# Kernel tuning notes

Hardware: AMD Instinct MI355X
Metric: run time of the kernel (lower is better)

Reference implementation:

```python
import jax, jax.numpy as jnp
import numpy as np

B, S, D, H, MLP, RH, RANK, BS, E, RES = 64, 197, 768, 12, 3072, 512, 256, 2, 3, 1
EPS = 1e-5


def _ln(x, g, b):
    m = jnp.mean(x, -1, keepdims=True)
    v = jnp.mean((x - m) ** 2, -1, keepdims=True)
    return (x - m) / jnp.sqrt(v + EPS) * g + b


def setup_inputs() -> dict:
    key = jax.random.key(0)
    ks = jax.random.split(key, 16)
    n = lambda k, shp, s: (jax.random.normal(k, shp) * s).astype(jnp.float32)
    inp = {
        'x': n(ks[0], (B, S, D), 1.0),
        'LRA_mask': jnp.arange(2 ** BS, dtype=jnp.int32),
        'wq_w': n(ks[1], (D, D), 0.02), 'wq_b': jnp.zeros((D,), jnp.float32),
        'wk_w': n(ks[2], (D, D), 0.02), 'wk_b': jnp.zeros((D,), jnp.float32),
        'wv_w': n(ks[3], (D, D), 0.02), 'wv_b': jnp.zeros((D,), jnp.float32),
        'wo_w': n(ks[4], (D, D), 0.02), 'wo_b': jnp.zeros((D,), jnp.float32),
        'an_g': jnp.ones((D,), jnp.float32), 'an_b': jnp.zeros((D,), jnp.float32),
        'fc1_w': n(ks[5], (MLP, D), 0.02), 'fc1_b': jnp.zeros((MLP,), jnp.float32),
        'fc2_w': n(ks[6], (D, MLP), 0.02), 'fc2_b': jnp.zeros((D,), jnp.float32),
        'fn_g': jnp.ones((D,), jnp.float32), 'fn_b': jnp.zeros((D,), jnp.float32),
        'r1_w': n(ks[7], (RH, D), 0.01), 'r1_b': jnp.zeros((RH,), jnp.float32),
        'rn_g': jnp.ones((RH,), jnp.float32), 'rn_b': jnp.zeros((RH,), jnp.float32),
        'r2_w': n(ks[8], (BS * 2, RH), 0.01),
        'r2_b': jnp.array([0.1, 5.0] * BS, jnp.float32),
        'eA': n(ks[9], (E, RANK, D), 0.01),  # down_proj weights [out=rank, in=dim]
        'eB': n(ks[10], (E, D, RANK), 0.01),  # up_proj weights [out=dim, in=rank]
    }
    return inp


def reference(x, LRA_mask, wq_w, wq_b, wk_w, wk_b, wv_w, wv_b, wo_w, wo_b,
              an_g, an_b, fc1_w, fc1_b, fc2_w, fc2_b, fn_g, fn_b,
              r1_w, r1_b, rn_g, rn_b, r2_w, r2_b, eA, eB):
    hd = D // H
    # ---- RouterModule (eval mode: argmax hard routing) on block input ----
    rlog = jax.nn.silu(_ln(x @ r1_w.T + r1_b, rn_g, rn_b)) @ r2_w.T + r2_b
    rlog = rlog.reshape(B, S, BS, 2)
    bits = jnp.argmax(rlog, -1)               # [B,S,BS], value of channel-1 one-hot
    bits = bits.at[:, :RES, :].set(1)          # reserved tokens -> full-one key (identity)
    pw = 2 ** jnp.arange(BS - 1, -1, -1)
    idx = jnp.sum(bits * pw, -1)               # [B,S] routing key per token
    # ---- Attention (pre-norm) ----
    h = _ln(x, an_g, an_b)
    q = (h @ wq_w.T + wq_b).reshape(B, S, H, hd).transpose(0, 2, 1, 3)
    k = (h @ wk_w.T + wk_b).reshape(B, S, H, hd).transpose(0, 2, 1, 3)
    v = (h @ wv_w.T + wv_b).reshape(B, S, H, hd).transpose(0, 2, 1, 3)
    att = jax.nn.softmax(jnp.einsum('bhqd,bhkd->bhqk', q, k) / np.float32(np.sqrt(hd)), -1)
    o = jnp.einsum('bhqk,bhkd->bhqd', att, v).transpose(0, 2, 1, 3).reshape(B, S, D)
    x1 = x + (o @ wo_w.T + wo_b)
    # ---- FeedForward (pre-norm, exact GELU like torch nn.GELU) ----
    x2 = x1 + (jax.nn.gelu(_ln(x1, fn_g, fn_b) @ fc1_w.T + fc1_b, approximate=False) @ fc2_w.T + fc2_b)
    # ---- BlockPathApproximators: disjoint per-key residual LoRA experts ----
    # keys 0..E-1 have experts; key 2^BS-1 (full-one) is identity. LRA_mask covers all keys.
    down = jnp.einsum('bsd,erd->bser', x2, eA)            # [B,S,E,RANK]
    up = jnp.einsum('bser,edr->bsed', down, eB)           # [B,S,E,D]
    sel = (idx[..., None] == jnp.arange(E)).astype(x2.dtype)  # one-hot over experts [B,S,E]
    out = x2 + jnp.einsum('bsed,bse->bsd', up, sel)
    return out
```

## Files before the change

### kernel.cpp

```cpp
#include <hip/hip_runtime.h>
#include <cstdint>

#define B_SZ   64
#define SEQ    197
#define DIM    768
#define NHEAD  12
#define HDK    64
#define MLP_D  3072
#define RH_D   512
#define RANK_D 256
#define NEXP   3
#define TOK    (B_SZ*SEQ)

typedef unsigned short u16;
typedef __attribute__((ext_vector_type(8))) short s16x8;
typedef __attribute__((ext_vector_type(4))) float f32x4;

static __device__ __forceinline__ u16 f2bf(float f) {
  unsigned u = __builtin_bit_cast(unsigned, f);
  u = u + 0x7FFFu + ((u >> 16) & 1u);
  return (u16)(u >> 16);
}

static __device__ __forceinline__ f32x4 mfma16(s16x8 a, s16x8 b, f32x4 c) {
  return __builtin_amdgcn_mfma_f32_16x16x32_bf16(a, b, c, 0, 0, 0);
}

static __device__ __forceinline__ void gload16(const u16* g, u16* l) {
  __builtin_amdgcn_global_load_lds(
      (const __attribute__((address_space(1))) unsigned int*)(const void*)g,
      (__attribute__((address_space(3))) unsigned int*)(void*)l,
      16, 0, 0);
}

static __device__ __forceinline__ float gelu_fast(float v) {
  const float u2 = 2.f * v * (0.7978845608f + 0.0356774081f * v * v);
  return v / (1.f + __expf(-u2));
}

__global__ void cvt_bf16(const float* __restrict__ in, u16* __restrict__ out, long n) {
  long i = ((long)blockIdx.x * blockDim.x + threadIdx.x) * 4;
  const long stride = (long)gridDim.x * blockDim.x * 4;
  for (; i < n; i += stride) {
    float4 v = *(const float4*)(in + i);
    unsigned r0 = (unsigned)f2bf(v.x) | ((unsigned)f2bf(v.y) << 16);
    unsigned r1 = (unsigned)f2bf(v.z) | ((unsigned)f2bf(v.w) << 16);
    *(uint2*)(out + i) = make_uint2(r0, r1);
  }
}

__global__ void concat3(const float* __restrict__ a, const float* __restrict__ b,
                        const float* __restrict__ c, float* __restrict__ out) {
  int i = blockIdx.x * 256 + threadIdx.x;
  if (i < DIM) { out[i] = a[i]; out[DIM + i] = b[i]; out[2*DIM + i] = c[i]; }
}

__global__ __launch_bounds__(256) void ln_rows(
    const float* __restrict__ x, const float* __restrict__ g,
    const float* __restrict__ bb, u16* __restrict__ out, int M)
{
  const int row = blockIdx.x * 4 + (threadIdx.x >> 6);
  const int lane = threadIdx.x & 63;
  if (row >= M) return;
  const float* xr = x + (long)row * DIM;
  float4 v[3];
  float s = 0.f, s2 = 0.f;
#pragma unroll
  for (int c = 0; c < 3; ++c) {
    v[c] = *(const float4*)(xr + c*256 + lane*4);
    s  += v[c].x + v[c].y + v[c].z + v[c].w;
    s2 += v[c].x*v[c].x + v[c].y*v[c].y + v[c].z*v[c].z + v[c].w*v[c].w;
  }
#pragma unroll
  for (int o = 1; o < 64; o <<= 1) { s += __shfl_xor(s, o); s2 += __shfl_xor(s2, o); }
  const float mean = s * (1.f/DIM);
  const float var  = s2 * (1.f/DIM) - mean*mean;
  const float rstd = rsqrtf(fmaxf(var, 0.f) + 1e-5f);
#pragma unroll
  for (int c = 0; c < 3; ++c) {
    const int idx = c*256 + lane*4;
    float4 gg = *(const float4*)(g + idx);
    float4 be = *(const float4*)(bb + idx);
    float y0 = (v[c].x - mean)*rstd*gg.x + be.x;
    float y1 = (v[c].y - mean)*rstd*gg.y + be.y;
    float y2 = (v[c].z - mean)*rstd*gg.z + be.z;
    float y3 = (v[c].w - mean)*rstd*gg.w + be.w;
    unsigned r0 = (unsigned)f2bf(y0) | ((unsigned)f2bf(y1) << 16);
    unsigned r1 = (unsigned)f2bf(y2) | ((unsigned)f2bf(y3) << 16);
    *(uint2*)(out + (long)row*DIM + idx) = make_uint2(r0, r1);
  }
}

template<int ACT, bool HAS_RES, bool OUT_F32, bool OUT_BF16>
__global__ __launch_bounds__(256, 3) void gemm_p3(
    const u16* __restrict__ A, const u16* __restrict__ Bm,
    const float* __restrict__ bias, const float* __restrict__ res,
    float* __restrict__ Cf, u16* __restrict__ Cb,
    int ldc, int M, int N, int K)
{
  __shared__ __align__(16) u16 lA[3][128*32];
  __shared__ __align__(16) u16 lB[3][128*32];
  const int tid  = threadIdx.x;
  const int lane = tid & 63;
  const int wave = tid >> 6;

  const int nwg  = gridDim.x * gridDim.y;
  const int orig = blockIdx.y * gridDim.x + blockIdx.x;
  const int xcd  = orig & 7;
  const int q    = nwg >> 3, r = nwg & 7;
  const int nb   = (xcd < r ? xcd * (q + 1) : r * (q + 1) + (xcd - r) * q) + (orig >> 3);
  const int m0 = (nb / gridDim.x) * 128;
  const int n0 = (nb % gridDim.x) * 128;

  const int fr = lane & 15, fg = lane >> 4;
  const int wr = wave >> 1, wc = wave & 1;

  const int srow  = tid >> 2;
  const int scol  = (((tid & 3) ^ ((tid >> 3) & 3)) & 3) * 8;
  const int r0a = m0 + srow, r1a = m0 + 64 + srow;
  const u16* pa0 = A  + (long)((r0a < M) ? r0a : M - 1) * K + scol;
  const u16* pa1 = A  + (long)((r1a < M) ? r1a : M - 1) * K + scol;
  const u16* pb0 = Bm + (long)(n0 + srow) * K + scol;
  const u16* pb1 = Bm + (long)(n0 + 64 + srow) * K + scol;
  const int soff = tid * 8;

  auto STAGE = [&](int b, int kt) {
    gload16(pa0 + kt, &lA[b][soff]);
    gload16(pa1 + kt, &lA[b][soff + 2048]);
    gload16(pb0 + kt, &lB[b][soff]);
    gload16(pb1 + kt, &lB[b][soff + 2048]);
  };

  const int abase = fr * 32 + (((fg ^ (fr >> 1)) & 3) << 3);

  f32x4 acc[4][4] = {};
  const int NT = K >> 5;

  STAGE(0, 0);
  STAGE(1, 32);

  int cur = 0;
#pragma unroll 1
  for (int t = 0; t < NT; ++t) {
    if (t < NT - 1) { asm volatile("s_waitcnt vmcnt(4)" ::: "memory"); }
    else           { asm volatile("s_waitcnt vmcnt(0)" ::: "memory"); }
    __builtin_amdgcn_s_barrier();
    if (t + 2 < NT) {
      int b2 = cur - 1; if (b2 < 0) b2 = 2;
      STAGE(b2, (t + 2) << 5);
    }
    s16x8 af[4], bfr[4];
#pragma unroll
    for (int m = 0; m < 4; ++m) af[m]  = *(const s16x8*)&lA[cur][wr*2048 + m*512 + abase];
#pragma unroll
    for (int n = 0; n < 4; ++n) bfr[n] = *(const s16x8*)&lB[cur][wc*2048 + n*512 + abase];
    asm volatile("s_waitcnt lgkmcnt(0)" ::: "memory");
    __builtin_amdgcn_sched_barrier(0);
    __builtin_amdgcn_s_setprio(1);
#pragma unroll
    for (int m = 0; m < 4; ++m)
#pragma unroll
      for (int n = 0; n < 4; ++n)
        acc[m][n] = mfma16(af[m], bfr[n], acc[m][n]);
    __builtin_amdgcn_s_setprio(0);
    cur = (cur == 2) ? 0 : cur + 1;
  }

#pragma unroll
  for (int m = 0; m < 4; ++m) {
#pragma unroll
    for (int n = 0; n < 4; ++n) {
      const int col = n0 + wc*64 + n*16 + fr;
      const float bv = bias[col];
#pragma unroll
      for (int r2 = 0; r2 < 4; ++r2) {
        const int row = m0 + wr*64 + m*16 + fg*4 + r2;
        if (row < M) {
          float v = acc[m][n][r2] + bv;
          if constexpr (ACT == 1) v = gelu_fast(v);
          if constexpr (HAS_RES) v += res[(long)row * N + col];
          if constexpr (OUT_F32) Cf[(long)row * ldc + col] = v;
          if constexpr (OUT_BF16) Cb[(long)row * ldc + col] = f2bf(v);
        }
      }
    }
  }
}

__global__ __launch_bounds__(256, 2) void attn(const u16* __restrict__ qkv, u16* __restrict__ o) {
  __shared__ __align__(16) u16 Vt[64][232];
  __shared__ __align__(16) u16 Pl[4][16][232];
  const int bh = blockIdx.x;
  const int b = bh / NHEAD, h = bh - b * NHEAD;
  const int tid = threadIdx.x, lane = tid & 63, wave = tid >> 6;
  const long rbase = (long)b * SEQ * 2304;

  for (int i = tid; i < 224*64; i += 256) {
    const int s = i >> 6, d = i & 63;
    u16 val = 0;
    if (s < SEQ) val = qkv[rbase + (long)s*2304 + 1536 + h*HDK + d];
    Vt[d][s] = val;
  }
  for (int i = lane; i < 16*24; i += 64) {
    Pl[wave][i / 24][208 + i % 24] = 0;
  }
  __syncthreads();

  const int fr = lane & 15, fg = lane >> 4;
  for (int qb = wave; qb < 13; qb += 4) {
    const int q0 = qb * 16;
    int qrow = q0 + fr; if (qrow > SEQ-1) qrow = SEQ-1;
    const u16* qp = qkv + rbase + (long)qrow*2304 + h*HDK;
    const s16x8 a0 = *(const s16x8*)(qp + fg*8);
    const s16x8 a1 = *(const s16x8*)(qp + 32 + fg*8);
    f32x4 sc[13];
    for (int kb = 0; kb < 13; ++kb) {
      int krow = kb*16 + fr; if (krow > SEQ-1) krow = SEQ-1;
      const u16* kp = qkv + rbase + (long)krow*2304 + DIM + h*HDK;
      const s16x8 b0 = *(const s16x8*)(kp + fg*8);
      const s16x8 b1 = *(const s16x8*)(kp + 32 + fg*8);
      f32x4 c = {0.f, 0.f, 0.f, 0.f};
      c = mfma16(a0, b0, c);
      c = mfma16(a1, b1, c);
      sc[kb] = c;
    }
    float inv[4];
#pragma unroll
    for (int r = 0; r < 4; ++r) {
      float mx = -3e38f;
      for (int kb = 0; kb < 13; ++kb) {
        const int col = kb*16 + fr;
        const float sv = sc[kb][r] * 0.125f;
        sc[kb][r] = sv;
        if (col < SEQ) mx = fmaxf(mx, sv);
      }
#pragma unroll
      for (int off = 1; off < 16; off <<= 1) mx = fmaxf(mx, __shfl_xor(mx, off));
      float sum = 0.f;
      for (int kb = 0; kb < 13; ++kb) {
        const int col = kb*16 + fr;
        const float p = (col < SEQ) ? __expf(sc[kb][r] - mx) : 0.f;
        sc[kb][r] = p;
        sum += p;
      }
#pragma unroll
      for (int off = 1; off < 16; off <<= 1) sum += __shfl_xor(sum, off);
      inv[r] = 1.f / sum;
    }
    asm volatile("s_waitcnt lgkmcnt(0)" ::: "memory");
    for (int kb = 0; kb < 13; ++kb) {
      const int col = kb*16 + fr;
#pragma unroll
      for (int r = 0; r < 4; ++r) Pl[wave][fg*4 + r][col] = f2bf(sc[kb][r]);
    }
    asm volatile("s_waitcnt lgkmcnt(0)" ::: "memory");
    for (int nb = 0; nb < 4; ++nb) {
      f32x4 acc = {0.f, 0.f, 0.f, 0.f};
#pragma unroll
      for (int kc = 0; kc < 7; ++kc) {
        const s16x8 pa = *(const s16x8*)&Pl[wave][fr][kc*32 + fg*8];
        const s16x8 vb = *(const s16x8*)&Vt[nb*16 + fr][kc*32 + fg*8];
        acc = mfma16(pa, vb, acc);
      }
#pragma unroll
      for (int r = 0; r < 4; ++r) {
        const int qr = q0 + fg*4 + r;
        if (qr < SEQ) o[((long)b*SEQ + qr)*DIM + h*HDK + nb*16 + fr] = f2bf(acc[r] * inv[r]);
      }
    }
  }
}

__global__ __launch_bounds__(64) void router_fin(
    const float* __restrict__ t1, const float* __restrict__ rg, const float* __restrict__ rb,
    const float* __restrict__ r2w, const float* __restrict__ r2b, int* __restrict__ idxb)
{
  const int t = blockIdx.x;
  const int lane = threadIdx.x;
  const float* row = t1 + (long)t * RH_D;
  float v[8];
  float s = 0.f, s2 = 0.f;
#pragma unroll
  for (int c = 0; c < 2; ++c) {
    float4 u = *(const float4*)(row + lane*8 + c*4);
    v[c*4+0]=u.x; v[c*4+1]=u.y; v[c*4+2]=u.z; v[c*4+3]=u.w;
    s += u.x+u.y+u.z+u.w;
    s2 += u.x*u.x+u.y*u.y+u.z*u.z+u.w*u.w;
  }
#pragma unroll
  for (int o = 1; o < 64; o <<= 1) { s += __shfl_xor(s, o); s2 += __shfl_xor(s2, o); }
  const float mean = s * (1.f/RH_D);
  const float var  = s2 * (1.f/RH_D) - mean*mean;
  const float rstd = rsqrtf(fmaxf(var, 0.f) + 1e-5f);
  float p[4] = {0.f, 0.f, 0.f, 0.f};
#pragma unroll
  for (int i = 0; i < 8; ++i) {
    const int col = lane*8 + i;
    float z = (v[i] - mean)*rstd*rg[col] + rb[col];
    z = z / (1.f + __expf(-z));
#pragma unroll
    for (int o = 0; o < 4; ++o) p[o] += z * r2w[o*RH_D + col];
  }
#pragma unroll
  for (int o = 0; o < 4; ++o)
#pragma unroll
    for (int off = 1; off < 64; off <<= 1) p[o] += __shfl_xor(p[o], off);
  if (lane == 0) {
    const float l0 = p[0]+r2b[0], l1 = p[1]+r2b[1], l2 = p[2]+r2b[2], l3 = p[3]+r2b[3];
    int b0 = (l1 > l0) ? 1 : 0;
    int b1 = (l3 > l2) ? 1 : 0;
    if (t % SEQ < 1) { b0 = 1; b1 = 1; }
    idxb[t] = b0*2 + b1;
  }
}

__global__ __launch_bounds__(256) void expert_apply(
    const int* __restrict__ idxb, const float* __restrict__ eA,
    const float* __restrict__ eB, float* __restrict__ out)
{
  const int t = blockIdx.x;
  const int e = idxb[t];
  if (e >= NEXP) return;
  __shared__ float xr[DIM];
  __shared__ float dn[RANK_D];
  const int tid = threadIdx.x;
  for (int i = tid; i < DIM; i += 256) xr[i] = out[(long)t*DIM + i];
  __syncthreads();
  {
    const float* ar = eA + ((long)e*RANK_D + tid)*DIM;
    float acc = 0.f;
    for (int k = 0; k < DIM; ++k) acc += ar[k]*xr[k];
    dn[tid] = acc;
  }
  __syncthreads();
  for (int d = tid; d < DIM; d += 256) {
    const float* br = eB + ((long)e*DIM + d)*RANK_D;
    float acc = 0.f;
    for (int r = 0; r < RANK_D; ++r) acc += br[r]*dn[r];
    out[(long)t*DIM + d] += acc;
  }
}

extern "C" void kernel_launch(void* const* d_in, const int* in_sizes, int n_in,
                              void* d_out, int out_size, void* d_ws, size_t ws_size,
                              hipStream_t stream) {
  (void)in_sizes; (void)n_in; (void)out_size;
  const float* x     = (const float*)d_in[0];
  const float* wq_w  = (const float*)d_in[2];
  const float* wq_b  = (const float*)d_in[3];
  const float* wk_w  = (const float*)d_in[4];
  const float* wk_b  = (const float*)d_in[5];
  const float* wv_w  = (const float*)d_in[6];
  const float* wv_b  = (const float*)d_in[7];
  const float* wo_w  = (const float*)d_in[8];
  const float* wo_b  = (const float*)d_in[9];
  const float* an_g  = (const float*)d_in[10];
  const float* an_b  = (const float*)d_in[11];
  const float* fc1_w = (const float*)d_in[12];
  const float* fc1_b = (const float*)d_in[13];
  const float* fc2_w = (const float*)d_in[14];
  const float* fc2_b = (const float*)d_in[15];
  const float* fn_g  = (const float*)d_in[16];
  const float* fn_b  = (const float*)d_in[17];
  const float* r1_w  = (const float*)d_in[18];
  const float* r1_b  = (const float*)d_in[19];
  const float* rn_g  = (const float*)d_in[20];
  const float* rn_b  = (const float*)d_in[21];
  const float* r2_w  = (const float*)d_in[22];
  const float* r2_b  = (const float*)d_in[23];
  const float* eA    = (const float*)d_in[24];
  const float* eB    = (const float*)d_in[25];
  float* outf = (float*)d_out;

  const size_t MiB = 1048576;
  const size_t NEED_FULL = 153*MiB;
  const size_t NEED_MIN  = 112*MiB + (size_t)TOK*DIM*2;
  if (ws_size < NEED_MIN) return;
  const bool full = (ws_size >= NEED_FULL);
  const int  nc   = full ? 1 : 2;
  const int  MC   = TOK / nc;
  const size_t offSY = full ? 94*MiB  : 72*MiB;
  const size_t offSZ = full ? 133*MiB : 112*MiB;

  char* ws = (char*)d_ws;
  u16*   Wqkv = (u16*)(ws + 0);
  u16*   Wo   = (u16*)(ws + 3538944);
  u16*   Wfc1 = (u16*)(ws + 4718592);
  u16*   Wfc2 = (u16*)(ws + 9437184);
  u16*   Wr1  = (u16*)(ws + 14155776);
  float* qkvb = (float*)(ws + 14942208);
  int*   idxb = (int*)(ws + 14952448);
  char* SX = ws + 16*MiB;
  char* SY = ws + offSY;
  char* SZ = ws + offSZ;
  u16*   x_b = (u16*)SX;
  u16*   qkv = (u16*)SX;
  u16*   m1  = (u16*)SX;
  float* t1  = (float*)SY;
  float* x1  = (float*)SY;
  u16*   h_b = (u16*)SZ;
  u16*   ob  = (u16*)SZ;
  u16*   h1  = (u16*)SZ;

  cvt_bf16<<<512, 256, 0, stream>>>(wq_w, Wqkv,               589824);
  cvt_bf16<<<512, 256, 0, stream>>>(wk_w, Wqkv + 589824,      589824);
  cvt_bf16<<<512, 256, 0, stream>>>(wv_w, Wqkv + 2*589824,    589824);
  cvt_bf16<<<512, 256, 0, stream>>>(wo_w, Wo,                 589824);
  cvt_bf16<<<1024, 256, 0, stream>>>(fc1_w, Wfc1,             2359296);
  cvt_bf16<<<1024, 256, 0, stream>>>(fc2_w, Wfc2,             2359296);
  cvt_bf16<<<512, 256, 0, stream>>>(r1_w, Wr1,                393216);
  cvt_bf16<<<2048, 256, 0, stream>>>(x, x_b,                  (long)TOK*DIM);
  concat3<<<3, 256, 0, stream>>>(wq_b, wk_b, wv_b, qkvb);

  gemm_p3<0, false, true, false><<<dim3(4, 99), 256, 0, stream>>>(
      x_b, Wr1, r1_b, nullptr, t1, nullptr, RH_D, TOK, RH_D, DIM);
  router_fin<<<TOK, 64, 0, stream>>>(t1, rn_g, rn_b, r2_w, r2_b, idxb);

  ln_rows<<<TOK/4, 256, 0, stream>>>(x, an_g, an_b, h_b, TOK);
  gemm_p3<0, false, false, true><<<dim3(18, 99), 256, 0, stream>>>(
      h_b, Wqkv, qkvb, nullptr, nullptr, qkv, 3*DIM, TOK, 3*DIM, DIM);
  attn<<<B_SZ*NHEAD, 256, 0, stream>>>(qkv, ob);
  gemm_p3<0, true, true, false><<<dim3(6, 99), 256, 0, stream>>>(
      ob, Wo, wo_b, x, x1, nullptr, DIM, TOK, DIM, DIM);

  ln_rows<<<TOK/4, 256, 0, stream>>>(x1, fn_g, fn_b, h1, TOK);
  for (int c = 0; c < nc; ++c) {
    const int r0 = c * MC;
    const int gy = (MC + 127) / 128;
    gemm_p3<1, false, false, true><<<dim3(24, gy), 256, 0, stream>>>(
        h1 + (long)r0*DIM, Wfc1, fc1_b, nullptr, nullptr, m1, MLP_D, MC, MLP_D, DIM);
    gemm_p3<0, true, true, false><<<dim3(6, gy), 256, 0, stream>>>(
        m1, Wfc2, fc2_b, x1 + (long)r0*DIM, outf + (long)r0*DIM, nullptr, DIM, MC, DIM, MLP_D);
  }

  expert_apply<<<TOK, 256, 0, stream>>>(idxb, eA, eB, outf);
}
```

Baseline: 504.5 us.

## Switch GEMM to double-buffered LDS pipeline and merge bf16 conversion kernels

Replaces the GEMM's three-stage LDS ring, which used explicit vmcnt waits, s_setprio and a sched barrier, with a simpler two-buffer scheme synchronised by __syncthreads each iteration, and drops the occupancy hint from launch bounds. It also folds the eight separate fp32-to-bf16 conversion launches into one kernel that picks source and destination by range. The merge cuts launch overhead. The GEMM change lowers LDS use per block but gives less prefetch depth and a full barrier per k-step, which may expose more load latency.

```diff
diff --git a/kernel.cpp b/kernel.cpp
--- a/kernel.cpp
+++ b/kernel.cpp
@@ -38,14 +38,29 @@
   return v / (1.f + __expf(-u2));
 }
 
-__global__ void cvt_bf16(const float* __restrict__ in, u16* __restrict__ out, long n) {
-  long i = ((long)blockIdx.x * blockDim.x + threadIdx.x) * 4;
-  const long stride = (long)gridDim.x * blockDim.x * 4;
-  for (; i < n; i += stride) {
-    float4 v = *(const float4*)(in + i);
+__global__ __launch_bounds__(256) void cvt_all(
+    const float* __restrict__ s0, const float* __restrict__ s1,
+    const float* __restrict__ s2, const float* __restrict__ s3,
+    const float* __restrict__ s4, const float* __restrict__ s5,
+    const float* __restrict__ s6, const float* __restrict__ s7,
+    u16* d0, u16* d1, u16* d2, u16* d3, u16* d4, u16* d5, u16* d6, u16* d7)
+{
+  const long T4 = 17154048L / 4;
+  for (long i = (long)blockIdx.x * 256 + threadIdx.x; i < T4; i += (long)gridDim.x * 256) {
+    const long e = i * 4;
+    const float* s; u16* d; long off;
+    if      (e < 589824L)   { s = s0; d = d0; off = e; }
+    else if (e < 1179648L)  { s = s1; d = d1; off = e - 589824L; }
+    else if (e < 1769472L)  { s = s2; d = d2; off = e - 1179648L; }
+    else if (e < 2359296L)  { s = s3; d = d3; off = e - 1769472L; }
+    else if (e < 4718592L)  { s = s4; d = d4; off = e - 2359296L; }
+    else if (e < 7077888L)  { s = s5; d = d5; off = e - 4718592L; }
+    else if (e < 7471104L)  { s = s6; d = d6; off = e - 7077888L; }
+    else                    { s = s7; d = d7; off = e - 7471104L; }
+    float4 v = *(const float4*)(s + off);
     unsigned r0 = (unsigned)f2bf(v.x) | ((unsigned)f2bf(v.y) << 16);
     unsigned r1 = (unsigned)f2bf(v.z) | ((unsigned)f2bf(v.w) << 16);
-    *(uint2*)(out + i) = make_uint2(r0, r1);
+    *(uint2*)(d + off) = make_uint2(r0, r1);
   }
 }
 
@@ -92,14 +107,14 @@
 }
 
 template<int ACT, bool HAS_RES, bool OUT_F32, bool OUT_BF16>
-__global__ __launch_bounds__(256, 3) void gemm_p3(
+__global__ __launch_bounds__(256) void gemm_db(
     const u16* __restrict__ A, const u16* __restrict__ Bm,
     const float* __restrict__ bias, const float* __restrict__ res,
     float* __restrict__ Cf, u16* __restrict__ Cb,
     int ldc, int M, int N, int K)
 {
-  __shared__ __align__(16) u16 lA[3][128*32];
-  __shared__ __align__(16) u16 lB[3][128*32];
+  __shared__ __align__(16) u16 lA[2][128*32];
+  __shared__ __align__(16) u16 lB[2][128*32];
   const int tid  = threadIdx.x;
   const int lane = tid & 63;
   const int wave = tid >> 6;
@@ -137,33 +152,23 @@
   const int NT = K >> 5;
 
   STAGE(0, 0);
-  STAGE(1, 32);
-
+  __syncthreads();
   int cur = 0;
 #pragma unroll 1
   for (int t = 0; t < NT; ++t) {
-    if (t < NT - 1) { asm volatile("s_waitcnt vmcnt(4)" ::: "memory"); }
-    else           { asm volatile("s_waitcnt vmcnt(0)" ::: "memory"); }
-    __builtin_amdgcn_s_barrier();
-    if (t + 2 < NT) {
-      int b2 = cur - 1; if (b2 < 0) b2 = 2;
-      STAGE(b2, (t + 2) << 5);
-    }
+    if (t + 1 < NT) STAGE(cur ^ 1, (t + 1) << 5);
     s16x8 af[4], bfr[4];
 #pragma unroll
     for (int m = 0; m < 4; ++m) af[m]  = *(const s16x8*)&lA[cur][wr*2048 + m*512 + abase];
 #pragma unroll
     for (int n = 0; n < 4; ++n) bfr[n] = *(const s16x8*)&lB[cur][wc*2048 + n*512 + abase];
-    asm volatile("s_waitcnt lgkmcnt(0)" ::: "memory");
-    __builtin_amdgcn_sched_barrier(0);
-    __builtin_amdgcn_s_setprio(1);
 #pragma unroll
     for (int m = 0; m < 4; ++m)
 #pragma unroll
       for (int n = 0; n < 4; ++n)
         acc[m][n] = mfma16(af[m], bfr[n], acc[m][n]);
-    __builtin_amdgcn_s_setprio(0);
-    cur = (cur == 2) ? 0 : cur + 1;
+    __syncthreads();
+    cur ^= 1;
   }
 
 #pragma unroll
@@ -402,34 +407,29 @@
   u16*   ob  = (u16*)SZ;
   u16*   h1  = (u16*)SZ;
 
-  cvt_bf16<<<512, 256, 0, stream>>>(wq_w, Wqkv,               589824);
-  cvt_bf16<<<512, 256, 0, stream>>>(wk_w, Wqkv + 589824,      589824);
-  cvt_bf16<<<512, 256, 0, stream>>>(wv_w, Wqkv + 2*589824,    589824);
-  cvt_bf16<<<512, 256, 0, stream>>>(wo_w, Wo,                 589824);
-  cvt_bf16<<<1024, 256, 0, stream>>>(fc1_w, Wfc1,             2359296);
-  cvt_bf16<<<1024, 256, 0, stream>>>(fc2_w, Wfc2,             2359296);
-  cvt_bf16<<<512, 256, 0, stream>>>(r1_w, Wr1,                393216);
-  cvt_bf16<<<2048, 256, 0, stream>>>(x, x_b,                  (long)TOK*DIM);
+  cvt_all<<<2048, 256, 0, stream>>>(
+      wq_w, wk_w, wv_w, wo_w, fc1_w, fc2_w, r1_w, x,
+      Wqkv, Wqkv + 589824, Wqkv + 2*589824, Wo, Wfc1, Wfc2, Wr1, x_b);
   concat3<<<3, 256, 0, stream>>>(wq_b, wk_b, wv_b, qkvb);
 
-  gemm_p3<0, false, true, false><<<dim3(4, 99), 256, 0, stream>>>(
+  gemm_db<0, false, true, false><<<dim3(4, 99), 256, 0, stream>>>(
       x_b, Wr1, r1_b, nullptr, t1, nullptr, RH_D, TOK, RH_D, DIM);
   router_fin<<<TOK, 64, 0, stream>>>(t1, rn_g, rn_b, r2_w, r2_b, idxb);
 
   ln_rows<<<TOK/4, 256, 0, stream>>>(x, an_g, an_b, h_b, TOK);
-  gemm_p3<0, false, false, true><<<dim3(18, 99), 256, 0, stream>>>(
+  gemm_db<0, false, false, true><<<dim3(18, 99), 256, 0, stream>>>(
       h_b, Wqkv, qkvb, nullptr, nullptr, qkv, 3*DIM, TOK, 3*DIM, DIM);
   attn<<<B_SZ*NHEAD, 256, 0, stream>>>(qkv, ob);
-  gemm_p3<0, true, true, false><<<dim3(6, 99), 256, 0, stream>>>(
+  gemm_db<0, true, true, false><<<dim3(6, 99), 256, 0, stream>>>(
       ob, Wo, wo_b, x, x1, nullptr, DIM, TOK, DIM, DIM);
 
   ln_rows<<<TOK/4, 256, 0, stream>>>(x1, fn_g, fn_b, h1, TOK);
   for (int c = 0; c < nc; ++c) {
     const int r0 = c * MC;
     const int gy = (MC + 127) / 128;
-    gemm_p3<1, false, false, true><<<dim3(24, gy), 256, 0, stream>>>(
+    gemm_db<1, false, false, true><<<dim3(24, gy), 256, 0, stream>>>(
         h1 + (long)r0*DIM, Wfc1, fc1_b, nullptr, nullptr, m1, MLP_D, MC, MLP_D, DIM);
-    gemm_p3<0, true, true, false><<<dim3(6, gy), 256, 0, stream>>>(
+    gemm_db<0, true, true, false><<<dim3(6, gy), 256, 0, stream>>>(
         m1, Wfc2, fc2_b, x1 + (long)r0*DIM, outf + (long)r0*DIM, nullptr, DIM, MC, DIM, MLP_D);
   }
 
```

Result: faster. 466.3 us (-7.6%).
